# Kernel tuning notes

Measured on AMD Instinct MI355X. Metric: run time of the kernel, lower is better.

The kernel has to match this reference:

```python
import jax, jax.numpy as jnp
import numpy as np

D_MODEL = 1024
H = 16
D_K = D_MODEL // H

def setup_inputs() -> dict:
    key = jax.random.key(0)
    ks = jax.random.split(key, 11)
    B, S = 2, 2048
    scale = 1.0 / np.sqrt(D_MODEL)
    inp = {
        'query': jax.random.normal(ks[0], (B, S, D_MODEL), jnp.float32),
        'key':   jax.random.normal(ks[1], (B, S, D_MODEL), jnp.float32),
        'value': jax.random.normal(ks[2], (B, S, D_MODEL), jnp.float32),
        'Wq': jax.random.normal(ks[3], (D_MODEL, D_MODEL), jnp.float32) * scale,
        'bq': jnp.zeros((D_MODEL,), jnp.float32),
        'Wk': jax.random.normal(ks[4], (D_MODEL, D_MODEL), jnp.float32) * scale,
        'bk': jnp.zeros((D_MODEL,), jnp.float32),
        'Wv': jax.random.normal(ks[5], (D_MODEL, D_MODEL), jnp.float32) * scale,
        'bv': jnp.zeros((D_MODEL,), jnp.float32),
        'Wo': jax.random.normal(ks[6], (D_MODEL, D_MODEL), jnp.float32) * scale,
        'bo': jnp.zeros((D_MODEL,), jnp.float32),
    }
    return inp

def reference(query, key, value, Wq, bq, Wk, bk, Wv, bv, Wo, bo):
    B, Sq, _ = query.shape
    # QKV projections, split into heads: [B,S,D] -> [B,H,S,d_k]
    def proj(x, W, b):
        y = x @ W.T + b
        return y.reshape(B, -1, H, D_K).transpose(0, 2, 1, 3)
    q = proj(query, Wq, bq)
    k = proj(key, Wk, bk)
    v = proj(value, Wv, bv)
    scores = jnp.einsum('bhqd,bhkd->bhqk', q, k) / jnp.sqrt(jnp.float32(D_K))
    attn = jax.nn.softmax(scores, axis=-1)  # [B,H,Sq,Sk]
    ctx = jnp.einsum('bhqk,bhkd->bhqd', attn, v)
    ctx = ctx.transpose(0, 2, 1, 3).reshape(B, Sq, D_MODEL)
    return ctx @ Wo.T + bo
```

## Files before the change

### kernel.cpp

```cpp
#include <hip/hip_runtime.h>
#include <cstdint>
#include <cmath>

typedef __attribute__((ext_vector_type(8))) __bf16 bf16x8;
typedef __attribute__((ext_vector_type(4))) __bf16 bf16x4;
typedef __attribute__((ext_vector_type(4))) float f32x4;

static constexpr float SM_C = 0.125f * 1.44269504088896340736f;

__device__ __forceinline__ float fast_exp2(float x) {
#if __has_builtin(__builtin_amdgcn_exp2f)
  return __builtin_amdgcn_exp2f(x);
#else
  return exp2f(x);
#endif
}

__device__ __forceinline__ f32x4 mfma16(bf16x8 a, bf16x8 b, f32x4 c) {
  return __builtin_amdgcn_mfma_f32_16x16x32_bf16(a, b, c, 0, 0, 0);
}

typedef __attribute__((address_space(1))) const void GVoid;
typedef __attribute__((address_space(3))) void LVoid;

__device__ __forceinline__ void load_lds16(const __bf16* g, __bf16* lds) {
  __builtin_amdgcn_global_load_lds((GVoid*)g, (LVoid*)lds, 16, 0, 0);
}

struct CvtArgs {
  const float* src[7];
  __bf16* dst[7];
  int n8[7];
};

__global__ __launch_bounds__(256) void cvt_kernel(CvtArgs args) {
  const int t = blockIdx.y;
  const float* s = args.src[t];
  __bf16* d = args.dst[t];
  const int n8 = args.n8[t];
  for (int i = blockIdx.x * 256 + threadIdx.x; i < n8; i += gridDim.x * 256) {
    float4 f0 = reinterpret_cast<const float4*>(s)[2 * i];
    float4 f1 = reinterpret_cast<const float4*>(s)[2 * i + 1];
    bf16x8 o;
    o[0] = (__bf16)f0.x; o[1] = (__bf16)f0.y; o[2] = (__bf16)f0.z; o[3] = (__bf16)f0.w;
    o[4] = (__bf16)f1.x; o[5] = (__bf16)f1.y; o[6] = (__bf16)f1.z; o[7] = (__bf16)f1.w;
    reinterpret_cast<bf16x8*>(d)[i] = o;
  }
}

__device__ __forceinline__ void gemm_tile_128(
    const __bf16* __restrict__ A, const __bf16* __restrict__ W,
    int m0, int n0, __bf16* A_lds, __bf16* B_lds, f32x4 acc[4][4])
{
  const int tid = threadIdx.x;
  const int l = tid & 63, l15 = l & 15, l4 = l >> 4;
  const int w = tid >> 6;
  const int wr = (w >> 1) * 64, wc = (w & 1) * 64;

  #pragma unroll 1
  for (int kt = 0; kt < 1024; kt += 64) {
    __syncthreads();
    #pragma unroll
    for (int c = 0; c < 4; ++c) {
      const int u = c * 256 + tid;
      const int row = u >> 3, ch = (u & 7) * 8;
      load_lds16(A + (size_t)(m0 + row) * 1024 + kt + ch, A_lds + u * 8);
      load_lds16(W + (size_t)(n0 + row) * 1024 + kt + ch, B_lds + u * 8);
    }
    __syncthreads();
    #pragma unroll
    for (int ks = 0; ks < 2; ++ks) {
      bf16x8 af[4], bw[4];
      #pragma unroll
      for (int i = 0; i < 4; ++i) {
        af[i] = *(const bf16x8*)(A_lds + (size_t)(wr + i * 16 + l15) * 64 + ks * 32 + l4 * 8);
        bw[i] = *(const bf16x8*)(B_lds + (size_t)(wc + i * 16 + l15) * 64 + ks * 32 + l4 * 8);
      }
      #pragma unroll
      for (int i = 0; i < 4; ++i)
        #pragma unroll
        for (int j = 0; j < 4; ++j)
          acc[i][j] = mfma16(af[i], bw[j], acc[i][j]);
    }
  }
}

__device__ __forceinline__ void xcd_swz_8x32(int& bx, int& by) {
  const int flat = by * 8 + bx;
  const int swz = (flat & 7) * 32 + (flat >> 3);
  bx = swz & 7; by = swz >> 3;
}

__global__ __launch_bounds__(256) void gemm_qkv(
    const __bf16* __restrict__ Xq, const __bf16* __restrict__ Xk, const __bf16* __restrict__ Xv,
    const __bf16* __restrict__ Wqb, const __bf16* __restrict__ Wkb, const __bf16* __restrict__ Wvb,
    const float* __restrict__ bq, const float* __restrict__ bk, const float* __restrict__ bv,
    __bf16* __restrict__ Qo, __bf16* __restrict__ Ko, __bf16* __restrict__ VTo)
{
  __shared__ __bf16 A_lds[128 * 64];
  __shared__ __bf16 B_lds[128 * 64];
  const int z = blockIdx.z;
  const __bf16* A = (z == 0) ? Xq : (z == 1) ? Xk : Xv;
  const __bf16* W = (z == 0) ? Wqb : (z == 1) ? Wkb : Wvb;
  const float* bias = (z == 0) ? bq : (z == 1) ? bk : bv;
  int bx = blockIdx.x, by = blockIdx.y;
  xcd_swz_8x32(bx, by);
  const int m0 = by * 128, n0 = bx * 128;

  f32x4 acc[4][4];
  const f32x4 z4 = {0.f, 0.f, 0.f, 0.f};
  #pragma unroll
  for (int i = 0; i < 4; ++i)
    #pragma unroll
    for (int j = 0; j < 4; ++j) acc[i][j] = z4;

  gemm_tile_128(A, W, m0, n0, A_lds, B_lds, acc);

  const int tid = threadIdx.x;
  const int l = tid & 63, l15 = l & 15, l4 = l >> 4;
  const int w = tid >> 6;
  const int wr = (w >> 1) * 64, wc = (w & 1) * 64;

  if (z < 2) {
    __bf16* C = (z == 0) ? Qo : Ko;
    const float cscale = (z == 0) ? SM_C : 1.0f;
    #pragma unroll
    for (int j = 0; j < 4; ++j) {
      const int n = n0 + wc + j * 16 + l15;
      const float bn = bias[n];
      #pragma unroll
      for (int i = 0; i < 4; ++i) {
        const int mbase = m0 + wr + i * 16 + 4 * l4;
        #pragma unroll
        for (int r = 0; r < 4; ++r)
          C[(size_t)(mbase + r) * 1024 + n] = (__bf16)((acc[i][j][r] + bn) * cscale);
      }
    }
  } else {
    #pragma unroll
    for (int j = 0; j < 4; ++j) {
      const int n = n0 + wc + j * 16 + l15;
      const float bn = bias[n];
      #pragma unroll
      for (int i = 0; i < 4; ++i) {
        const int mbase = m0 + wr + i * 16 + 4 * l4;
        bf16x4 v;
        #pragma unroll
        for (int r = 0; r < 4; ++r) v[r] = (__bf16)(acc[i][j][r] + bn);
        *(bf16x4*)(VTo + (size_t)n * 4096 + mbase) = v;
      }
    }
  }
}

__global__ __launch_bounds__(256) void gemm_out_k(
    const __bf16* __restrict__ CTXb, const __bf16* __restrict__ Wob,
    const float* __restrict__ bo, float* __restrict__ out)
{
  __shared__ __bf16 A_lds[128 * 64];
  __shared__ __bf16 B_lds[128 * 64];
  int bx = blockIdx.x, by = blockIdx.y;
  xcd_swz_8x32(bx, by);
  const int m0 = by * 128, n0 = bx * 128;

  f32x4 acc[4][4];
  const f32x4 z4 = {0.f, 0.f, 0.f, 0.f};
  #pragma unroll
  for (int i = 0; i < 4; ++i)
    #pragma unroll
    for (int j = 0; j < 4; ++j) acc[i][j] = z4;

  gemm_tile_128(CTXb, Wob, m0, n0, A_lds, B_lds, acc);

  const int tid = threadIdx.x;
  const int l = tid & 63, l15 = l & 15, l4 = l >> 4;
  const int w = tid >> 6;
  const int wr = (w >> 1) * 64, wc = (w & 1) * 64;

  #pragma unroll
  for (int j = 0; j < 4; ++j) {
    const int n = n0 + wc + j * 16 + l15;
    const float bn = bo[n];
    #pragma unroll
    for (int i = 0; i < 4; ++i) {
      const int mbase = m0 + wr + i * 16 + 4 * l4;
      #pragma unroll
      for (int r = 0; r < 4; ++r)
        out[(size_t)(mbase + r) * 1024 + n] = acc[i][j][r] + bn;
    }
  }
}

__global__ __launch_bounds__(256, 2) void attn_kernel(
    const __bf16* __restrict__ Q, const __bf16* __restrict__ K,
    const __bf16* __restrict__ VT, __bf16* __restrict__ CTX)
{
  __shared__ __bf16 Kl[2][64][72];
  __shared__ __bf16 Vl[2][64][72];
  __shared__ __bf16 Pl[4][32][80];

  const int tid = threadIdx.x;
  const int w = tid >> 6, l = tid & 63, l15 = l & 15, l4 = l >> 4;
  const int bid = blockIdx.x;
  const int qt = bid >> 5, pair = bid & 31, h = pair & 15, b = pair >> 4;
  const int q0 = qt * 128 + w * 32;

  const int sr0 = tid >> 3, sc0 = (tid & 7) * 8;
  const int sr1 = (tid + 256) >> 3, sc1 = (tid & 7) * 8;

  const __bf16* Kbase = K + (size_t)b * 2048 * 1024 + h * 64;
  const __bf16* VTbase = VT + (size_t)(h * 64) * 4096 + (size_t)b * 2048;

  const __bf16* Qbase = Q + (size_t)(b * 2048 + q0) * 1024 + h * 64;
  bf16x8 qa[2][2];
  #pragma unroll
  for (int qf = 0; qf < 2; ++qf)
    #pragma unroll
    for (int df = 0; df < 2; ++df)
      qa[qf][df] = *(const bf16x8*)(Qbase + (size_t)(qf * 16 + l15) * 1024 + df * 32 + l4 * 8);

  f32x4 ctxa[2][4];
  const f32x4 z4 = {0.f, 0.f, 0.f, 0.f};
  #pragma unroll
  for (int qf = 0; qf < 2; ++qf)
    #pragma unroll
    for (int nf = 0; nf < 4; ++nf) ctxa[qf][nf] = z4;

  f32x4 lacc[2] = {z4, z4};

  bf16x8 kst0, kst1, vst0, vst1;
  kst0 = *(const bf16x8*)(Kbase + (size_t)sr0 * 1024 + sc0);
  kst1 = *(const bf16x8*)(Kbase + (size_t)sr1 * 1024 + sc1);
  vst0 = *(const bf16x8*)(VTbase + (size_t)sr0 * 4096 + sc0);
  vst1 = *(const bf16x8*)(VTbase + (size_t)sr1 * 4096 + sc1);

  #pragma unroll 1
  for (int kv = 0; kv < 32; ++kv) {
    const int buf = kv & 1;
    *(bf16x8*)&Kl[buf][sr0][sc0] = kst0;
    *(bf16x8*)&Kl[buf][sr1][sc1] = kst1;
    *(bf16x8*)&Vl[buf][sr0][sc0] = vst0;
    *(bf16x8*)&Vl[buf][sr1][sc1] = vst1;
    __syncthreads();

    if (kv < 31) {
      const int s = (kv + 1) * 64;
      kst0 = *(const bf16x8*)(Kbase + (size_t)(s + sr0) * 1024 + sc0);
      kst1 = *(const bf16x8*)(Kbase + (size_t)(s + sr1) * 1024 + sc1);
      vst0 = *(const bf16x8*)(VTbase + (size_t)sr0 * 4096 + s + sc0);
      vst1 = *(const bf16x8*)(VTbase + (size_t)sr1 * 4096 + s + sc1);
    }

    bf16x8 kb[2][4];
    #pragma unroll
    for (int df = 0; df < 2; ++df)
      #pragma unroll
      for (int kf = 0; kf < 4; ++kf)
        kb[df][kf] = *(const bf16x8*)&Kl[buf][kf * 16 + l15][df * 32 + l4 * 8];
    f32x4 sacc[2][4];
    #pragma unroll
    for (int qf = 0; qf < 2; ++qf)
      #pragma unroll
      for (int kf = 0; kf < 4; ++kf) sacc[qf][kf] = z4;
    __builtin_amdgcn_s_setprio(1);
    #pragma unroll
    for (int df = 0; df < 2; ++df)
      #pragma unroll
      for (int qf = 0; qf < 2; ++qf)
        #pragma unroll
        for (int kf = 0; kf < 4; ++kf)
          sacc[qf][kf] = mfma16(kb[df][kf], qa[qf][df], sacc[qf][kf]);
    __builtin_amdgcn_s_setprio(0);

    bf16x8 va[4][2];
    #pragma unroll
    for (int nf = 0; nf < 4; ++nf)
      #pragma unroll
      for (int ks = 0; ks < 2; ++ks)
        va[nf][ks] = *(const bf16x8*)&Vl[buf][nf * 16 + l15][ks * 32 + l4 * 8];

    #pragma unroll
    for (int qf = 0; qf < 2; ++qf)
      #pragma unroll
      for (int kf = 0; kf < 4; ++kf) {
        bf16x4 pw;
        #pragma unroll
        for (int r = 0; r < 4; ++r) {
          const float p = fast_exp2(sacc[qf][kf][r]);
          lacc[qf][r] += p;
          pw[r] = (__bf16)p;
        }
        *(bf16x4*)&Pl[w][qf * 16 + l15][kf * 16 + 4 * l4] = pw;
      }

    asm volatile("" ::: "memory");

    bf16x8 pb[2][2];
    #pragma unroll
    for (int qf = 0; qf < 2; ++qf)
      #pragma unroll
      for (int ks = 0; ks < 2; ++ks)
        pb[qf][ks] = *(const bf16x8*)&Pl[w][qf * 16 + l15][ks * 32 + 8 * l4];
    __builtin_amdgcn_s_setprio(1);
    #pragma unroll
    for (int ks = 0; ks < 2; ++ks)
      #pragma unroll
      for (int qf = 0; qf < 2; ++qf)
        #pragma unroll
        for (int nf = 0; nf < 4; ++nf)
          ctxa[qf][nf] = mfma16(va[nf][ks], pb[qf][ks], ctxa[qf][nf]);
    __builtin_amdgcn_s_setprio(0);
  }

  __bf16* Cb = CTX + (size_t)(b * 2048 + q0) * 1024 + h * 64;
  #pragma unroll
  for (int qf = 0; qf < 2; ++qf) {
    float l_ = (lacc[qf][0] + lacc[qf][1]) + (lacc[qf][2] + lacc[qf][3]);
    l_ += __shfl_xor(l_, 16);
    l_ += __shfl_xor(l_, 32);
    const float inv = 1.0f / l_;
    #pragma unroll
    for (int nf = 0; nf < 4; ++nf) {
      bf16x4 o;
      #pragma unroll
      for (int r = 0; r < 4; ++r) o[r] = (__bf16)(ctxa[qf][nf][r] * inv);
      *(bf16x4*)(Cb + (size_t)(qf * 16 + l15) * 1024 + nf * 16 + 4 * l4) = o;
    }
  }
}

extern "C" void kernel_launch(void* const* d_in, const int* in_sizes, int n_in,
                              void* d_out, int out_size, void* d_ws, size_t ws_size,
                              hipStream_t stream) {
  (void)in_sizes; (void)n_in; (void)out_size; (void)ws_size;
  const float* query = (const float*)d_in[0];
  const float* key_  = (const float*)d_in[1];
  const float* value = (const float*)d_in[2];
  const float* Wq = (const float*)d_in[3];
  const float* bq = (const float*)d_in[4];
  const float* Wk = (const float*)d_in[5];
  const float* bk = (const float*)d_in[6];
  const float* Wv = (const float*)d_in[7];
  const float* bv = (const float*)d_in[8];
  const float* Wo = (const float*)d_in[9];
  const float* bo = (const float*)d_in[10];
  float* out = (float*)d_out;

  char* ws = (char*)d_ws;
  const size_t MB = 1ull << 20;
  __bf16* Xq  = (__bf16*)(ws + 0 * MB);
  __bf16* Xk  = (__bf16*)(ws + 8 * MB);
  __bf16* Xv  = (__bf16*)(ws + 16 * MB);
  __bf16* Wqb = (__bf16*)(ws + 24 * MB);
  __bf16* Wkb = (__bf16*)(ws + 26 * MB);
  __bf16* Wvb = (__bf16*)(ws + 28 * MB);
  __bf16* Wob = (__bf16*)(ws + 30 * MB);
  __bf16* Qb  = (__bf16*)(ws + 32 * MB);
  __bf16* Kb  = (__bf16*)(ws + 40 * MB);
  __bf16* VTb = (__bf16*)(ws + 48 * MB);
  __bf16* CTXb= (__bf16*)(ws + 56 * MB);

  CvtArgs ca;
  ca.src[0] = query; ca.dst[0] = Xq;  ca.n8[0] = 4096 * 1024 / 8;
  ca.src[1] = key_;  ca.dst[1] = Xk;  ca.n8[1] = 4096 * 1024 / 8;
  ca.src[2] = value; ca.dst[2] = Xv;  ca.n8[2] = 4096 * 1024 / 8;
  ca.src[3] = Wq;    ca.dst[3] = Wqb; ca.n8[3] = 1024 * 1024 / 8;
  ca.src[4] = Wk;    ca.dst[4] = Wkb; ca.n8[4] = 1024 * 1024 / 8;
  ca.src[5] = Wv;    ca.dst[5] = Wvb; ca.n8[5] = 1024 * 1024 / 8;
  ca.src[6] = Wo;    ca.dst[6] = Wob; ca.n8[6] = 1024 * 1024 / 8;
  cvt_kernel<<<dim3(1024, 7), dim3(256), 0, stream>>>(ca);

  gemm_qkv<<<dim3(8, 32, 3), dim3(256), 0, stream>>>(
      Xq, Xk, Xv, Wqb, Wkb, Wvb, bq, bk, bv, Qb, Kb, VTb);

  attn_kernel<<<dim3(512), dim3(256), 0, stream>>>(Qb, Kb, VTb, CTXb);

  gemm_out_k<<<dim3(8, 32), dim3(256), 0, stream>>>(CTXb, Wob, bo, out);
}
```

Before: 140.9 us.

## Double-buffer GEMM LDS tiles with register prefetch and padded rows

Replaces the direct global-to-LDS loads in the shared 128x128 GEMM tile loop with register-staged prefetch. The next K tile is loaded from global memory while MFMAs run on the current one, and the LDS tiles are double-buffered, so one barrier per iteration suffices. LDS rows are padded to a stride of 72 to reduce bank conflicts on the fragment reads, and launch bounds request 2 blocks per CU. The cost is more LDS per block (about 72KB), extra VGPRs for the staged data, and an extra LDS write pass.

```diff
diff --git a/kernel.cpp b/kernel.cpp
--- a/kernel.cpp
+++ b/kernel.cpp
@@ -18,13 +18,6 @@
 
 __device__ __forceinline__ f32x4 mfma16(bf16x8 a, bf16x8 b, f32x4 c) {
   return __builtin_amdgcn_mfma_f32_16x16x32_bf16(a, b, c, 0, 0, 0);
-}
-
-typedef __attribute__((address_space(1))) const void GVoid;
-typedef __attribute__((address_space(3))) void LVoid;
-
-__device__ __forceinline__ void load_lds16(const __bf16* g, __bf16* lds) {
-  __builtin_amdgcn_global_load_lds((GVoid*)g, (LVoid*)lds, 16, 0, 0);
 }
 
 struct CvtArgs {
@@ -48,6 +41,9 @@
   }
 }
 
+#define LDS_STRIDE 72
+#define LDS_TILE (128 * LDS_STRIDE)
+
 __device__ __forceinline__ void gemm_tile_128(
     const __bf16* __restrict__ A, const __bf16* __restrict__ W,
     int m0, int n0, __bf16* A_lds, __bf16* B_lds, f32x4 acc[4][4])
@@ -56,25 +52,42 @@
   const int l = tid & 63, l15 = l & 15, l4 = l >> 4;
   const int w = tid >> 6;
   const int wr = (w >> 1) * 64, wc = (w & 1) * 64;
+  const int srow = tid >> 3, sch = (tid & 7) * 8;
+
+  bf16x8 ast[4], bst[4];
+  #pragma unroll
+  for (int c = 0; c < 4; ++c) {
+    ast[c] = *(const bf16x8*)(A + (size_t)(m0 + c * 32 + srow) * 1024 + sch);
+    bst[c] = *(const bf16x8*)(W + (size_t)(n0 + c * 32 + srow) * 1024 + sch);
+  }
 
   #pragma unroll 1
-  for (int kt = 0; kt < 1024; kt += 64) {
+  for (int it = 0; it < 16; ++it) {
+    __bf16* Al = A_lds + (it & 1) * LDS_TILE;
+    __bf16* Bl = B_lds + (it & 1) * LDS_TILE;
+    #pragma unroll
+    for (int c = 0; c < 4; ++c) {
+      *(bf16x8*)(Al + (size_t)(c * 32 + srow) * LDS_STRIDE + sch) = ast[c];
+      *(bf16x8*)(Bl + (size_t)(c * 32 + srow) * LDS_STRIDE + sch) = bst[c];
+    }
     __syncthreads();
-    #pragma unroll
-    for (int c = 0; c < 4; ++c) {
-      const int u = c * 256 + tid;
-      const int row = u >> 3, ch = (u & 7) * 8;
-      load_lds16(A + (size_t)(m0 + row) * 1024 + kt + ch, A_lds + u * 8);
-      load_lds16(W + (size_t)(n0 + row) * 1024 + kt + ch, B_lds + u * 8);
-    }
-    __syncthreads();
+
+    if (it < 15) {
+      const int kt = (it + 1) * 64;
+      #pragma unroll
+      for (int c = 0; c < 4; ++c) {
+        ast[c] = *(const bf16x8*)(A + (size_t)(m0 + c * 32 + srow) * 1024 + kt + sch);
+        bst[c] = *(const bf16x8*)(W + (size_t)(n0 + c * 32 + srow) * 1024 + kt + sch);
+      }
+    }
+
     #pragma unroll
     for (int ks = 0; ks < 2; ++ks) {
       bf16x8 af[4], bw[4];
       #pragma unroll
       for (int i = 0; i < 4; ++i) {
-        af[i] = *(const bf16x8*)(A_lds + (size_t)(wr + i * 16 + l15) * 64 + ks * 32 + l4 * 8);
-        bw[i] = *(const bf16x8*)(B_lds + (size_t)(wc + i * 16 + l15) * 64 + ks * 32 + l4 * 8);
+        af[i] = *(const bf16x8*)(Al + (size_t)(wr + i * 16 + l15) * LDS_STRIDE + ks * 32 + l4 * 8);
+        bw[i] = *(const bf16x8*)(Bl + (size_t)(wc + i * 16 + l15) * LDS_STRIDE + ks * 32 + l4 * 8);
       }
       #pragma unroll
       for (int i = 0; i < 4; ++i)
@@ -91,14 +104,14 @@
   bx = swz & 7; by = swz >> 3;
 }
 
-__global__ __launch_bounds__(256) void gemm_qkv(
+__global__ __launch_bounds__(256, 2) void gemm_qkv(
     const __bf16* __restrict__ Xq, const __bf16* __restrict__ Xk, const __bf16* __restrict__ Xv,
     const __bf16* __restrict__ Wqb, const __bf16* __restrict__ Wkb, const __bf16* __restrict__ Wvb,
     const float* __restrict__ bq, const float* __restrict__ bk, const float* __restrict__ bv,
     __bf16* __restrict__ Qo, __bf16* __restrict__ Ko, __bf16* __restrict__ VTo)
 {
-  __shared__ __bf16 A_lds[128 * 64];
-  __shared__ __bf16 B_lds[128 * 64];
+  __shared__ __bf16 A_lds[2 * LDS_TILE];
+  __shared__ __bf16 B_lds[2 * LDS_TILE];
   const int z = blockIdx.z;
   const __bf16* A = (z == 0) ? Xq : (z == 1) ? Xk : Xv;
   const __bf16* W = (z == 0) ? Wqb : (z == 1) ? Wkb : Wvb;
@@ -153,12 +166,12 @@
   }
 }
 
-__global__ __launch_bounds__(256) void gemm_out_k(
+__global__ __launch_bounds__(256, 2) void gemm_out_k(
     const __bf16* __restrict__ CTXb, const __bf16* __restrict__ Wob,
     const float* __restrict__ bo, float* __restrict__ out)
 {
-  __shared__ __bf16 A_lds[128 * 64];
-  __shared__ __bf16 B_lds[128 * 64];
+  __shared__ __bf16 A_lds[2 * LDS_TILE];
+  __shared__ __bf16 B_lds[2 * LDS_TILE];
   int bx = blockIdx.x, by = blockIdx.y;
   xcd_swz_8x32(bx, by);
   const int m0 = by * 128, n0 = bx * 128;
```

Result: faster. 120.7 us (-14.4%).
